# Optimization experiments

Measured on AMD Instinct MI355X. Metric: run time of the kernel, lower is better.

Reference implementation:

```python
import jax, jax.numpy as jnp
import numpy as np
from jax import lax

THRESH = 0.6      # pnet score threshold (threshold[0])
IOU_THR = 0.5     # per-scale nms threshold in detect_face
K_PICKS = 128     # fixed max number of NMS picks (jit-static)
STRIDE = 2.0
CELL = 12.0
NEG = -1e30


def _conv(x, w, b):
    y = lax.conv_general_dilated(x, w, (1, 1), 'VALID',
                                 dimension_numbers=('NCHW', 'OIHW', 'NCHW'))
    return y + b[None, :, None, None]


def _prelu(x, a):
    return jnp.where(x > 0, x, a[None, :, None, None] * x)


def _maxpool2(x):
    return lax.reduce_window(x, -jnp.inf, lax.max, (1, 1, 2, 2), (1, 1, 2, 2), 'VALID')


def _nms(boxes, scores):
    # Greedy union-IoU NMS (nms_numpy math), vectorized with a fixed pick budget.
    # boxes [N,4] (shared grid), scores [N] with invalid entries already = NEG.
    x1, y1, x2, y2 = boxes[:, 0], boxes[:, 1], boxes[:, 2], boxes[:, 3]
    area = (x2 - x1 + 1.0) * (y2 - y1 + 1.0)

    def body(live, _):
        j = jnp.argmax(live)
        s = live[j]
        ok = s > NEG * 0.5
        xx1 = jnp.maximum(x1[j], x1); yy1 = jnp.maximum(y1[j], y1)
        xx2 = jnp.minimum(x2[j], x2); yy2 = jnp.minimum(y2[j], y2)
        inter = jnp.maximum(0.0, xx2 - xx1 + 1.0) * jnp.maximum(0.0, yy2 - yy1 + 1.0)
        iou = inter / (area[j] + area - inter)
        live = jnp.where(iou > IOU_THR, NEG, live).at[j].set(NEG)
        return live, (j, ok)

    _, (idx, ok) = lax.scan(body, scores, None, length=K_PICKS)
    return idx, ok


def setup_inputs():
    key = jax.random.key(0)
    ks = jax.random.split(key, 16)
    B, H, W = 16, 384, 512
    f = lambda k, shp, s=0.1: jax.random.normal(k, shp, jnp.float32) * s
    return {
        'im_data': jax.random.uniform(ks[0], (B, 3, H, W), jnp.float32) * 255.0,
        'c1_w': f(ks[1], (10, 3, 3, 3)), 'c1_b': f(ks[2], (10,)),
        'p1': jnp.full((10,), 0.25, jnp.float32),
        'c2_w': f(ks[3], (16, 10, 3, 3)), 'c2_b': f(ks[4], (16,)),
        'p2': jnp.full((16,), 0.25, jnp.float32),
        'c3_w': f(ks[5], (32, 16, 3, 3)), 'c3_b': f(ks[6], (32,)),
        'p3': jnp.full((32,), 0.25, jnp.float32),
        'c41_w': f(ks[7], (2, 32, 1, 1)), 'c41_b': f(ks[8], (2,)),
        'c42_w': f(ks[9], (4, 32, 1, 1)), 'c42_b': f(ks[10], (4,)),
    }


def reference(im_data, c1_w, c1_b, p1, c2_w, c2_b, p2, c3_w, c3_b, p3,
              c41_w, c41_b, c42_w, c42_b):
    # --- PNet conv trunk (detect_face normalization + MTCNN PNet) ---
    x = (im_data - 127.5) * 0.0078125
    h = _prelu(_conv(x, c1_w, c1_b), p1)
    h = _maxpool2(h)                                   # 2x2 s2 (dims even -> ceil==floor)
    h = _prelu(_conv(h, c2_w, c2_b), p2)
    h = _prelu(_conv(h, c3_w, c3_b), p3)
    probs = jax.nn.softmax(_conv(h, c41_w, c41_b), axis=1)[:, 1]   # [B,Hp,Wp]
    reg = _conv(h, c42_w, c42_b)                                   # [B,4,Hp,Wp]

    # --- generateBoundingBox (dense, masked instead of nonzero; scale=1) ---
    B, Hp, Wp = probs.shape
    yy, xx = jnp.meshgrid(jnp.arange(Hp, dtype=jnp.float32),
                          jnp.arange(Wp, dtype=jnp.float32), indexing='ij')
    boxes4 = jnp.stack([jnp.floor(STRIDE * xx + 1.0).ravel(),
                        jnp.floor(STRIDE * yy + 1.0).ravel(),
                        jnp.floor(STRIDE * xx + CELL).ravel(),
                        jnp.floor(STRIDE * yy + CELL).ravel()], axis=1)  # [N,4]
    scores = probs.reshape(B, -1)                                   # [B,N]
    regf = reg.reshape(B, 4, -1).transpose(0, 2, 1)                 # [B,N,4]
    masked = jnp.where(scores >= THRESH, scores, NEG)

    # --- per-image greedy NMS (batched_nms: images independent) ---
    idx, ok = jax.vmap(_nms, in_axes=(None, 0))(boxes4, masked)     # [B,K]
    pb = boxes4[idx]                                                # [B,K,4]
    ps = jnp.take_along_axis(scores, idx, axis=1)                   # [B,K]
    pr = jnp.take_along_axis(regf, idx[..., None], axis=1)          # [B,K,4]

    w = pb[..., 2] - pb[..., 0]
    hh = pb[..., 3] - pb[..., 1]
    q1 = pb[..., 0] + pr[..., 0] * w
    q2 = pb[..., 1] + pr[..., 1] * hh
    q3 = pb[..., 2] + pr[..., 2] * w
    q4 = pb[..., 3] + pr[..., 3] * hh
    rw = q3 - q1
    rh = q4 - q2
    l = jnp.maximum(rw, rh)
    nx1 = q1 + rw * 0.5 - l * 0.5
    ny1 = q2 + rh * 0.5 - l * 0.5
    out = jnp.stack([nx1, ny1, nx1 + l, ny1 + l, ps], axis=-1)      # [B,K,5]
    return out * ok[..., None].astype(out.dtype)
```

## Files before the change

### kernel.cpp

```cpp
#include <hip/hip_runtime.h>
#include <math.h>

#define BATCH 16
#define IH 384
#define IW 512
#define C1 10
#define P1H 191
#define P1W 255
#define C2 16
#define H2 189
#define W2 253
#define C3 32
#define H3 187
#define W3 251
#define N3 (H3*W3)
#define KP 128
#define CAP 7680
#define NEGV (-1e30f)

typedef _Float16 f16x8 __attribute__((ext_vector_type(8)));
typedef _Float16 f16x4 __attribute__((ext_vector_type(4)));
typedef float    f32x16 __attribute__((ext_vector_type(16)));

#define PXT 66
#define NSUB 2

#define T1R 34
#define T1C 68
__global__ __launch_bounds__(256, 2) void k_conv1pool(
        const float* __restrict__ im, const float* __restrict__ w,
        const float* __restrict__ bia, const float* __restrict__ slope,
        float* __restrict__ outp,
        const float* __restrict__ w3, _Float16* __restrict__ wbuf) {
    __shared__ float T[3 * T1R * T1C];

    int tx = threadIdx.x, ty = threadIdx.y;
    int tid = ty * 16 + tx;
    int bx = blockIdx.x, by = blockIdx.y, bb = blockIdx.z;

    if (bx == 0 && by == 0 && bb == 0) {
        for (int e = tid; e < 4608; e += 256) {
            int oc = e / 144;
            int rem = e - oc * 144;
            int ic = rem / 9;
            int tap = rem - ic * 9;
            float v = w3[e];
            _Float16 h = (_Float16)v;
            _Float16 l = (_Float16)(v - (float)h);
            int d = ((tap * 2 + (ic >> 3)) * 32 + oc) * 8 + (ic & 7);
            wbuf[d] = h;
            wbuf[4608 + d] = l;
        }
    }

    const size_t ibase = (size_t)bb * 3 * IH * IW;
    for (int g = tid; g < 3 * T1R * 33; g += 256) {
        int ch = g / (T1R * 33);
        int rem = g - ch * (T1R * 33);
        int r = rem / 33;
        int c2 = rem - r * 33;
        int yg = 32 * by + r;
        int xg = 64 * bx + 2 * c2;
        float2 v = make_float2(0.f, 0.f);
        if (yg < IH && xg < IW)
            v = *(const float2*)(im + ibase + ((size_t)ch * IH + yg) * IW + xg);
        float2 o;
        o.x = (v.x - 127.5f) * 0.0078125f;
        o.y = (v.y - 127.5f) * 0.0078125f;
        *(float2*)&T[(ch * T1R + r) * T1C + 2 * c2] = o;
    }
    __syncthreads();

    int Y  = by * 16 + ty;
    int X0 = bx * 32 + 2 * tx;
    if (Y >= P1H) return;

    float win[3][4][6];
    #pragma unroll
    for (int ch = 0; ch < 3; ++ch)
        #pragma unroll
        for (int r = 0; r < 4; ++r) {
            const float* p = &T[(ch * T1R + 2 * ty + r) * T1C + 4 * tx];
            float4 a = *(const float4*)p;
            float2 b = *(const float2*)(p + 4);
            win[ch][r][0] = a.x; win[ch][r][1] = a.y;
            win[ch][r][2] = a.z; win[ch][r][3] = a.w;
            win[ch][r][4] = b.x; win[ch][r][5] = b.y;
        }

    bool px1ok = (X0 + 1 < P1W);
    for (int oc = 0; oc < C1; ++oc) {
        const float* wo = w + oc * 27;
        float bv = bia[oc], sv = slope[oc];
        float c0 = bv, c1 = bv, c2 = bv, c3 = bv;
        float c4 = bv, c5 = bv, c6 = bv, c7 = bv;
        #pragma unroll
        for (int ch = 0; ch < 3; ++ch)
            #pragma unroll
            for (int ky = 0; ky < 3; ++ky)
                #pragma unroll
                for (int kx = 0; kx < 3; ++kx) {
                    float wv = wo[(ch * 3 + ky) * 3 + kx];
                    c0 += win[ch][0 + ky][0 + kx] * wv;
                    c1 += win[ch][0 + ky][1 + kx] * wv;
                    c2 += win[ch][0 + ky][2 + kx] * wv;
                    c3 += win[ch][0 + ky][3 + kx] * wv;
                    c4 += win[ch][1 + ky][0 + kx] * wv;
                    c5 += win[ch][1 + ky][1 + kx] * wv;
                    c6 += win[ch][1 + ky][2 + kx] * wv;
                    c7 += win[ch][1 + ky][3 + kx] * wv;
                }
        float m0 = fmaxf(fmaxf(c0, c1), fmaxf(c4, c5));
        float m1 = fmaxf(fmaxf(c2, c3), fmaxf(c6, c7));
        float p0 = m0 > 0.f ? m0 : sv * m0;
        float p1 = m1 > 0.f ? m1 : sv * m1;
        float* o = outp + (((size_t)bb * C1 + oc) * P1H + Y) * P1W + X0;
        o[0] = p0;
        if (px1ok) o[1] = p1;
    }
}

__global__ __launch_bounds__(256, 2) void k_conv2(
        const float* __restrict__ inp, const float* __restrict__ w,
        const float* __restrict__ bia, const float* __restrict__ slope,
        float* __restrict__ outp) {
    __shared__ float4 sbuf[2048];
    int tx = threadIdx.x, ty = threadIdx.y;
    int tid = ty * 64 + tx;
    int x0 = blockIdx.x * 128 + tx * 2;
    int y  = blockIdx.y * 4 + ty;
    int bb = blockIdx.z;
    bool alive = (x0 < W2) && (y < H2);

    float a0[C2], a1[C2];
    #pragma unroll
    for (int oc = 0; oc < C2; ++oc) { a0[oc] = bia[oc]; a1[oc] = bia[oc]; }

    if (alive) {
        bool tail = (x0 + 3 > P1W - 1);
        for (int ci = 0; ci < C1; ++ci) {
            const float* p = inp + (((size_t)bb * C1 + ci) * P1H + y) * P1W + x0;
            float v[3][4];
            #pragma unroll
            for (int r = 0; r < 3; ++r) {
                const float* pr = p + (size_t)r * P1W;
                v[r][0] = pr[0]; v[r][1] = pr[1]; v[r][2] = pr[2];
                v[r][3] = tail ? 0.f : pr[3];
            }
            const float* wc = w + ci * 9;
            #pragma unroll
            for (int oc = 0; oc < C2; ++oc) {
                const float* wo = wc + oc * (C1 * 9);
                float s0 = a0[oc], s1 = a1[oc];
                #pragma unroll
                for (int ky = 0; ky < 3; ++ky)
                    #pragma unroll
                    for (int kx = 0; kx < 3; ++kx) {
                        float wv = wo[ky * 3 + kx];
                        s0 += v[ky][kx]     * wv;
                        s1 += v[ky][kx + 1] * wv;
                    }
                a0[oc] = s0; a1[oc] = s1;
            }
        }
        #pragma unroll
        for (int oc = 0; oc < C2; ++oc) {
            float sl = slope[oc];
            float u0 = a0[oc]; a0[oc] = u0 > 0.f ? u0 : sl * u0;
            float u1 = a1[oc]; a1[oc] = u1 > 0.f ? u1 : sl * u1;
        }
    }

    #pragma unroll
    for (int c4 = 0; c4 < 4; ++c4) {
        int g0 = tid * 8 + c4;
        int p0 = g0 ^ ((g0 >> 3) & 7);
        sbuf[p0] = make_float4(a0[c4 * 4], a0[c4 * 4 + 1], a0[c4 * 4 + 2], a0[c4 * 4 + 3]);
        int g1 = tid * 8 + 4 + c4;
        int p1 = g1 ^ ((g1 >> 3) & 7);
        sbuf[p1] = make_float4(a1[c4 * 4], a1[c4 * 4 + 1], a1[c4 * 4 + 2], a1[c4 * 4 + 3]);
    }
    __syncthreads();

    const size_t obase = (size_t)bb * H2 * W2 * C2;
    #pragma unroll
    for (int it = 0; it < 8; ++it) {
        int g = it * 256 + tid;
        int c4 = g & 3, px = (g >> 2) & 127, ry = g >> 9;
        int xg = blockIdx.x * 128 + px, yg = blockIdx.y * 4 + ry;
        if (xg < W2 && yg < H2) {
            int phys = g ^ ((g >> 3) & 7);
            *(float4*)(outp + obase + ((size_t)yg * W2 + xg) * C2 + c4 * 4) = sbuf[phys];
        }
    }
}

__global__ __launch_bounds__(256, 2) void k_conv3mfma(
        const float* __restrict__ act,
        const _Float16* __restrict__ wbuf,
        const float* __restrict__ b3, const float* __restrict__ s3,
        const float* __restrict__ w41, const float* __restrict__ b41,
        const float* __restrict__ w42, const float* __restrict__ b42,
        float* __restrict__ scores, float4* __restrict__ regf) {
    __shared__ __align__(16) _Float16 Ah[6 * 2 * PXT * 8];
    __shared__ __align__(16) _Float16 Al[6 * 2 * PXT * 8];
    __shared__ __align__(16) float    htab[32 * 8];

    int tid = threadIdx.x;
    int bx = blockIdx.x * (NSUB * 32);
    int by = blockIdx.y * 4;
    int bb = blockIdx.z;

    {
        int oc = tid >> 3, f = tid & 7;
        float v;
        if      (f == 0) v = b3[oc];
        else if (f == 1) v = s3[oc];
        else if (f == 2) v = w41[oc];
        else if (f == 3) v = w41[32 + oc];
        else             v = w42[(f - 4) * 32 + oc];
        htab[tid] = v;
    }
    {
        const float* actb = act + (size_t)bb * H2 * W2 * C2;
        for (int e = tid; e < 6 * PXT * 4; e += 256) {
            int ic4 = e & 3;
            int t = e >> 2;
            int px = t % PXT;
            int row = t / PXT;
            int yg = by + row, xg = bx + px;
            float4 v = make_float4(0.f, 0.f, 0.f, 0.f);
            if (yg < H2 && xg < W2)
                v = *(const float4*)(actb + ((size_t)yg * W2 + xg) * C2 + ic4 * 4);
            float xs0 = v.x, xs1 = v.y, xs2 = v.z, xs3 = v.w;
            f16x4 hv, lv;
            _Float16 h;
            h = (_Float16)xs0; hv[0] = h; lv[0] = (_Float16)(xs0 - (float)h);
            h = (_Float16)xs1; hv[1] = h; lv[1] = (_Float16)(xs1 - (float)h);
            h = (_Float16)xs2; hv[2] = h; lv[2] = (_Float16)(xs2 - (float)h);
            h = (_Float16)xs3; hv[3] = h; lv[3] = (_Float16)(xs3 - (float)h);
            int kg = ic4 >> 1, h4 = ic4 & 1;
            int gr = (row * 2 + kg) * PXT + px;
            *(f16x4*)(Ah + gr * 8 + h4 * 4) = hv;
            *(f16x4*)(Al + gr * 8 + h4 * 4) = lv;
        }
    }
    __syncthreads();

    int wv = tid >> 6, lane = tid & 63;
    int col = lane & 31, half = lane >> 5;
    int y = by + wv;
    if (y >= H3) return;

    f32x16 acc[NSUB];
    #pragma unroll
    for (int s = 0; s < NSUB; ++s)
        #pragma unroll
        for (int i = 0; i < 16; ++i) acc[s][i] = 0.f;

    const _Float16* wg = wbuf + (half * 32 + col) * 8;

    #pragma unroll 1
    for (int ky = 0; ky < 3; ++ky) {
        const _Float16* arh = Ah + ((wv + ky) * 2 + half) * (PXT * 8);
        const _Float16* arl = Al + ((wv + ky) * 2 + half) * (PXT * 8);
        #pragma unroll
        for (int kx = 0; kx < 3; ++kx) {
            int tap = ky * 3 + kx;
            f16x8 wh = *(const f16x8*)(wg + tap * 512);
            f16x8 wl = *(const f16x8*)(wg + 4608 + tap * 512);
            #pragma unroll
            for (int s = 0; s < NSUB; ++s) {
                int p = s * 32 + col + kx;
                f16x8 bh = *(const f16x8*)(arh + p * 8);
                f16x8 bl = *(const f16x8*)(arl + p * 8);
                acc[s] = __builtin_amdgcn_mfma_f32_32x32x16_f16(wh, bh, acc[s], 0, 0, 0);
                acc[s] = __builtin_amdgcn_mfma_f32_32x32x16_f16(wl, bh, acc[s], 0, 0, 0);
                acc[s] = __builtin_amdgcn_mfma_f32_32x32x16_f16(wh, bl, acc[s], 0, 0, 0);
            }
        }
    }

    float L0[NSUB], L1[NSUB], R0[NSUB], R1[NSUB], R2[NSUB], R3[NSUB];
    #pragma unroll
    for (int s = 0; s < NSUB; ++s) { L0[s]=0.f; L1[s]=0.f; R0[s]=0.f; R1[s]=0.f; R2[s]=0.f; R3[s]=0.f; }

    #pragma unroll
    for (int r = 0; r < 16; ++r) {
        int oc = (r & 3) + 8 * (r >> 2) + 4 * half;
        float4 t0 = *(const float4*)&htab[oc * 8];
        float4 t1 = *(const float4*)&htab[oc * 8 + 4];
        #pragma unroll
        for (int s = 0; s < NSUB; ++s) {
            float v = acc[s][r] + t0.x;
            v = v > 0.f ? v : v * t0.y;
            L0[s] += v * t0.z; L1[s] += v * t0.w;
            R0[s] += v * t1.x; R1[s] += v * t1.y;
            R2[s] += v * t1.z; R3[s] += v * t1.w;
        }
    }

    float hb0 = b41[0], hb1 = b41[1];
    float rb0 = b42[0], rb1 = b42[1], rb2 = b42[2], rb3 = b42[3];

    #pragma unroll
    for (int s = 0; s < NSUB; ++s) {
        float l0 = L0[s] + __shfl_xor(L0[s], 32) + hb0;
        float l1 = L1[s] + __shfl_xor(L1[s], 32) + hb1;
        float r0 = R0[s] + __shfl_xor(R0[s], 32) + rb0;
        float r1 = R1[s] + __shfl_xor(R1[s], 32) + rb1;
        float r2 = R2[s] + __shfl_xor(R2[s], 32) + rb2;
        float r3 = R3[s] + __shfl_xor(R3[s], 32) + rb3;
        float m = fmaxf(l0, l1);
        float e0 = expf(l0 - m), e1 = expf(l1 - m);
        float p = e1 / (e0 + e1);
        int px = bx + s * 32 + col;
        if (half == 0 && px < W3) {
            size_t n = (size_t)bb * N3 + (size_t)y * W3 + px;
            scores[n] = (p >= 0.6f) ? p : NEGV;
            regf[n] = make_float4(r0, r1, r2, r3);
        }
    }
}

__global__ __launch_bounds__(1024) void k_nms(
        const float* __restrict__ scores, const float4* __restrict__ regf,
        float* __restrict__ outp) {
    __shared__ float s_score[CAP];
    __shared__ int   s_idx[CAP];
    __shared__ float r_s[16];
    __shared__ int   r_i[16];
    __shared__ float s_picks[KP];
    __shared__ int   s_picki[KP];
    __shared__ int   s_misc[4];

    int tid = threadIdx.x;
    int bb = blockIdx.x;
    const float* sc = scores + (size_t)bb * N3;

    if (tid < 4) s_misc[tid] = 0;
    __syncthreads();

    int cnt = 0;
    for (int i = tid; i < N3; i += 1024) if (sc[i] > 0.f) cnt++;
    atomicAdd(&s_misc[0], cnt);
    __syncthreads();
    int M = s_misc[0];

    int cutbin = 0;
    if (M > CAP) {
        for (int i = tid; i < 2048; i += 1024) s_idx[i] = 0;
        __syncthreads();
        for (int i = tid; i < N3; i += 1024) {
            float s = sc[i];
            if (s > 0.f) {
                int b = (int)((s - 0.6f) * 5120.f);
                b = b < 0 ? 0 : (b > 2047 ? 2047 : b);
                atomicAdd(&s_idx[b], 1);
            }
        }
        __syncthreads();
        if (tid == 0) {
            int accum = 0, b = 2047;
            for (; b >= 0; --b) {
                int c = s_idx[b];
                if (accum + c > CAP) break;
                accum += c;
            }
            s_misc[2] = b + 1;
        }
        __syncthreads();
        cutbin = s_misc[2];
        __syncthreads();
    }

    for (int i = tid; i < N3; i += 1024) {
        float s = sc[i];
        if (s > 0.f) {
            bool keep = true;
            if (M > CAP) {
                int b = (int)((s - 0.6f) * 5120.f);
                b = b < 0 ? 0 : (b > 2047 ? 2047 : b);
                keep = (b >= cutbin);
            }
            if (keep) {
                int pos = atomicAdd(&s_misc[1], 1);
                if (pos < CAP) { s_score[pos] = s; s_idx[pos] = i; }
            }
        }
    }
    __syncthreads();
    int M2 = s_misc[1]; if (M2 > CAP) M2 = CAP;

    int np = 0;
    for (int pick = 0; pick < KP; ++pick) {
        float bs = -INFINITY; int bi = 0x7fffffff;
        for (int i = tid; i < M2; i += 1024) {
            float s = s_score[i]; int id = s_idx[i];
            if (s > bs || (s == bs && id < bi)) { bs = s; bi = id; }
        }
        #pragma unroll
        for (int off = 32; off; off >>= 1) {
            float os = __shfl_down(bs, off);
            int   oi = __shfl_down(bi, off);
            if (os > bs || (os == bs && oi < bi)) { bs = os; bi = oi; }
        }
        int lane = tid & 63, wv = tid >> 6;
        if (lane == 0) { r_s[wv] = bs; r_i[wv] = bi; }
        __syncthreads();
        if (tid == 0) {
            float ps = r_s[0]; int pi = r_i[0];
            for (int k = 1; k < 16; ++k) {
                float os = r_s[k]; int oi = r_i[k];
                if (os > ps || (os == ps && oi < pi)) { ps = os; pi = oi; }
            }
            s_picks[pick] = ps; s_picki[pick] = pi;
            r_s[0] = ps; r_i[0] = pi;
        }
        __syncthreads();
        float ps = r_s[0]; int pi = r_i[0];
        if (ps < 0.f) break;
        np = pick + 1;

        int pcx = pi % W3, pcy = pi / W3;
        float px1 = (float)(2 * pcx + 1), py1 = (float)(2 * pcy + 1);
        float px2 = (float)(2 * pcx + 12), py2 = (float)(2 * pcy + 12);
        for (int i = tid; i < M2; i += 1024) {
            float s = s_score[i];
            if (s > NEGV * 0.5f) {
                int id = s_idx[i];
                int cx = id % W3, cy = id / W3;
                float x1 = (float)(2 * cx + 1), y1 = (float)(2 * cy + 1);
                float x2 = (float)(2 * cx + 12), y2 = (float)(2 * cy + 12);
                float xx1 = fmaxf(px1, x1), yy1 = fmaxf(py1, y1);
                float xx2 = fminf(px2, x2), yy2 = fminf(py2, y2);
                float inter = fmaxf(0.f, xx2 - xx1 + 1.f) * fmaxf(0.f, yy2 - yy1 + 1.f);
                float iou = inter / (288.f - inter);
                if (iou > 0.5f) s_score[i] = NEGV;
            }
        }
        __syncthreads();
    }

    if (tid < KP) {
        float* o = outp + ((size_t)bb * KP + tid) * 5;
        if (tid < np) {
            int pi = s_picki[tid]; float ps = s_picks[tid];
            int cx = pi % W3, cy = pi / W3;
            float x1 = (float)(2 * cx + 1), y1 = (float)(2 * cy + 1);
            float x2 = (float)(2 * cx + 12), y2 = (float)(2 * cy + 12);
            float4 r = regf[(size_t)bb * N3 + pi];
            float wd = x2 - x1, hh = y2 - y1;
            float q1 = x1 + r.x * wd, q2 = y1 + r.y * hh;
            float q3 = x2 + r.z * wd, q4 = y2 + r.w * hh;
            float rw = q3 - q1, rh = q4 - q2;
            float L = fmaxf(rw, rh);
            float nx1 = q1 + rw * 0.5f - L * 0.5f;
            float ny1 = q2 + rh * 0.5f - L * 0.5f;
            o[0] = nx1; o[1] = ny1; o[2] = nx1 + L; o[3] = ny1 + L; o[4] = ps;
        } else {
            o[0] = 0.f; o[1] = 0.f; o[2] = 0.f; o[3] = 0.f; o[4] = 0.f;
        }
    }
}

extern "C" void kernel_launch(void* const* d_in, const int* in_sizes, int n_in,
                              void* d_out, int out_size, void* d_ws, size_t ws_size,
                              hipStream_t stream) {
    const float* im   = (const float*)d_in[0];
    const float* c1w  = (const float*)d_in[1];
    const float* c1b  = (const float*)d_in[2];
    const float* p1   = (const float*)d_in[3];
    const float* c2w  = (const float*)d_in[4];
    const float* c2b  = (const float*)d_in[5];
    const float* p2   = (const float*)d_in[6];
    const float* c3w  = (const float*)d_in[7];
    const float* c3b  = (const float*)d_in[8];
    const float* p3   = (const float*)d_in[9];
    const float* c41w = (const float*)d_in[10];
    const float* c41b = (const float*)d_in[11];
    const float* c42w = (const float*)d_in[12];
    const float* c42b = (const float*)d_in[13];

    float* ws = (float*)d_ws;
    const size_t POOL1_FLOATS = (size_t)BATCH * C1 * P1H * P1W;
    float*  pool1  = ws;
    float*  conv2b = ws + POOL1_FLOATS;
    float*  scoresb = ws;
    float4* regfb   = (float4*)(ws + (size_t)BATCH * N3);
    _Float16* wbuf = (_Float16*)d_out;

    k_conv1pool<<<dim3(8, 12, BATCH), dim3(16, 16), 0, stream>>>(im, c1w, c1b, p1, pool1,
                                                                 c3w, wbuf);
    k_conv2   <<<dim3(2, 48, BATCH), dim3(64, 4), 0, stream>>>(pool1, c2w, c2b, p2, conv2b);
    k_conv3mfma<<<dim3(4, 47, BATCH), dim3(256), 0, stream>>>(conv2b, wbuf, c3b, p3,
                                                              c41w, c41b, c42w, c42b,
                                                              scoresb, regfb);
    k_nms<<<dim3(BATCH), dim3(1024), 0, stream>>>(scoresb, regfb, (float*)d_out);
}
```

Baseline: 234.8 us.

## Stage conv2 input tile in LDS and pin conv1 window registers

conv2 now loads a 10-channel 6x130 input halo tile into shared memory cooperatively, then reads its 3x4 windows from LDS instead of from global memory per thread. The shared buffer is reused for the output transpose, which adds an extra barrier. conv1pool drops its occupancy hint from 2 to 1 blocks per SIMD and uses empty asm statements to keep the input window in VGPRs, aiming to stop the compiler from rematerialising LDS loads. The trade-off is lower occupancy for conv1 and added LDS traffic and sync for conv2.

```diff
diff --git a/kernel.cpp b/kernel.cpp
--- a/kernel.cpp
+++ b/kernel.cpp
@@ -27,7 +27,7 @@
 
 #define T1R 34
 #define T1C 68
-__global__ __launch_bounds__(256, 2) void k_conv1pool(
+__global__ __launch_bounds__(256, 1) void k_conv1pool(
         const float* __restrict__ im, const float* __restrict__ w,
         const float* __restrict__ bia, const float* __restrict__ slope,
         float* __restrict__ outp,
@@ -87,6 +87,13 @@
             win[ch][r][2] = a.z; win[ch][r][3] = a.w;
             win[ch][r][4] = b.x; win[ch][r][5] = b.y;
         }
+    #pragma unroll
+    for (int ch = 0; ch < 3; ++ch)
+        #pragma unroll
+        for (int r = 0; r < 4; ++r)
+            #pragma unroll
+            for (int c = 0; c < 6; ++c)
+                asm volatile("" : "+v"(win[ch][r][c]));
 
     bool px1ok = (X0 + 1 < P1W);
     for (int oc = 0; oc < C1; ++oc) {
@@ -124,12 +131,31 @@
         const float* __restrict__ inp, const float* __restrict__ w,
         const float* __restrict__ bia, const float* __restrict__ slope,
         float* __restrict__ outp) {
-    __shared__ float4 sbuf[2048];
+    __shared__ __align__(16) float smem[8192];
+    float* tile = smem;
+    float4* sbuf = (float4*)smem;
+
     int tx = threadIdx.x, ty = threadIdx.y;
     int tid = ty * 64 + tx;
-    int x0 = blockIdx.x * 128 + tx * 2;
-    int y  = blockIdx.y * 4 + ty;
-    int bb = blockIdx.z;
+    int bx = blockIdx.x, byb = blockIdx.y, bb = blockIdx.z;
+
+    const float* pin = inp + (size_t)bb * C1 * P1H * P1W;
+    for (int g = tid; g < C1 * 6 * 130; g += 256) {
+        int ic = g / 780;
+        int rem = g - ic * 780;
+        int r = rem / 130;
+        int c = rem - r * 130;
+        int yg = 4 * byb + r;
+        int xg = 128 * bx + c;
+        float v = 0.f;
+        if (yg < P1H && xg < P1W)
+            v = pin[((size_t)ic * P1H + yg) * P1W + xg];
+        tile[(ic * 6 + r) * 132 + c] = v;
+    }
+    __syncthreads();
+
+    int x0 = bx * 128 + tx * 2;
+    int y  = byb * 4 + ty;
     bool alive = (x0 < W2) && (y < H2);
 
     float a0[C2], a1[C2];
@@ -137,15 +163,14 @@
     for (int oc = 0; oc < C2; ++oc) { a0[oc] = bia[oc]; a1[oc] = bia[oc]; }
 
     if (alive) {
-        bool tail = (x0 + 3 > P1W - 1);
         for (int ci = 0; ci < C1; ++ci) {
-            const float* p = inp + (((size_t)bb * C1 + ci) * P1H + y) * P1W + x0;
             float v[3][4];
             #pragma unroll
             for (int r = 0; r < 3; ++r) {
-                const float* pr = p + (size_t)r * P1W;
-                v[r][0] = pr[0]; v[r][1] = pr[1]; v[r][2] = pr[2];
-                v[r][3] = tail ? 0.f : pr[3];
+                const float* p = &tile[(ci * 6 + ty + r) * 132 + 2 * tx];
+                float2 u0 = *(const float2*)p;
+                float2 u1 = *(const float2*)(p + 2);
+                v[r][0] = u0.x; v[r][1] = u0.y; v[r][2] = u1.x; v[r][3] = u1.y;
             }
             const float* wc = w + ci * 9;
             #pragma unroll
@@ -170,6 +195,7 @@
             float u1 = a1[oc]; a1[oc] = u1 > 0.f ? u1 : sl * u1;
         }
     }
+    __syncthreads();
 
     #pragma unroll
     for (int c4 = 0; c4 < 4; ++c4) {
```

Result: slower. 249.4 us (+6.2%).
